# Optimization experiments

Measured on AMD Instinct MI355X. Metric: run time of the kernel, lower is better.

The kernel has to match this reference:

```python
import jax, jax.numpy as jnp
import numpy as np

N_NODES = 40000
N_EDGES = 640000
DIM = 128
N_BASIS = 50
N_FILTERS = 128
CUTOFF = 5.0
LOG2 = float(np.log(2.0))
PI = float(np.pi)


def ssp(t):
    # ShiftedSoftplus: softplus(x) - log(2), numerically stable via logaddexp
    return jnp.logaddexp(t, 0.0) - LOG2


def setup_inputs() -> dict:
    key = jax.random.key(0)
    ks = jax.random.split(key, 16)
    u = lambda k, shape, fan_in: jax.random.uniform(k, shape, jnp.float32, -1.0, 1.0) / np.sqrt(fan_in)
    return {
        "x": jax.random.normal(ks[0], (N_NODES, DIM), jnp.float32),
        "r_ij": jax.random.uniform(ks[1], (N_EDGES,), jnp.float32) * CUTOFF,
        "f_ij": jax.random.normal(ks[2], (N_EDGES, N_BASIS), jnp.float32),
        "ind_i": jax.random.randint(ks[3], (N_EDGES,), 0, N_NODES),
        "ind_j": jax.random.randint(ks[4], (N_EDGES,), 0, N_NODES),
        # parameters
        "W_in2f": u(ks[5], (DIM, N_FILTERS), DIM),            # Linear(dim, n_filters, bias=False)
        "W_f1": u(ks[6], (N_BASIS, N_FILTERS), N_BASIS),       # filter_network Linear 1
        "b_f1": u(ks[7], (N_FILTERS,), N_BASIS),
        "W_f2": u(ks[8], (N_FILTERS, N_FILTERS), N_FILTERS),   # filter_network Linear 2
        "b_f2": u(ks[9], (N_FILTERS,), N_FILTERS),
        "W_out": u(ks[10], (N_FILTERS, DIM), N_FILTERS),       # f2out Linear
        "b_out": u(ks[11], (DIM,), N_FILTERS),
        "W_lin": u(ks[12], (DIM, DIM), DIM),                   # final lin
        "b_lin": u(ks[13], (DIM,), DIM),
    }


def reference(x, r_ij, f_ij, ind_i, ind_j,
              W_in2f, W_f1, b_f1, W_f2, b_f2, W_out, b_out, W_lin, b_lin):
    # filter network: Linear -> ShiftedSoftplus -> Linear, on edges: [E, nf]
    W = ssp(f_ij @ W_f1 + b_f1) @ W_f2 + b_f2
    # cosine cutoff: [E]
    C = 0.5 * (jnp.cos(r_ij * (PI / CUTOFF)) + 1.0) * (r_ij < CUTOFF).astype(r_ij.dtype)
    W = W * C[:, None]
    # node embedding -> filters: [N, nf]
    h = x @ W_in2f
    # gather source nodes, modulate by filters: [E, nf]
    msg = h[ind_j] * W
    # scatter-add pool to destination nodes: [N, nf]
    agg = jax.ops.segment_sum(msg, ind_i, num_segments=x.shape[0])
    # f2out: Linear -> ShiftedSoftplus, then final Linear
    v = ssp(agg @ W_out + b_out)
    return v @ W_lin + b_lin
```

## Files before the change

kernel.cpp:

```cpp
#include <hip/hip_runtime.h>
#include <hip/hip_fp16.h>

#define N_NODES_C 40000
#define N_EDGES_C 640000
#define DIM 128
#define NB 50
#define LDA 132
#define BLK 256
#define TROWS 64
#define LOG2_C 0.6931471805599453f
#define PI_OVER_CUT 0.6283185307179586f
#define NSCAN_BLK 157

typedef __attribute__((ext_vector_type(8))) short s8v;
typedef __attribute__((ext_vector_type(4))) float f4v;

#define MFMA_BF16 __builtin_amdgcn_mfma_f32_16x16x32_bf16

#define SEG_IN2F_H 0
#define SEG_IN2F_L 20480
#define SEG_F1_H   40960
#define SEG_F1_L   51200
#define SEG_F2_H   61440
#define SEG_F2_L   81920
#define SEG_OUT_H  102400
#define SEG_OUT_L  122880
#define SEG_LIN_H  143360
#define SEG_LIN_L  163840
#define WSPLIT_USHORTS 184320

__device__ __forceinline__ unsigned short f2bf(float x) {
    unsigned int u = __float_as_uint(x);
    u += 0x7fffu + ((u >> 16) & 1u);
    return (unsigned short)(u >> 16);
}
__device__ __forceinline__ float bf2f(unsigned short h) {
    return __uint_as_float(((unsigned int)h) << 16);
}
__device__ __forceinline__ float ssp_f(float t) {
    float e = __expf(-fabsf(t));
    return fmaxf(t, 0.0f) + __logf(1.0f + e) - LOG2_C;
}
__device__ __forceinline__ void split8t(const float* av, s8v& Ah, s8v& Al) {
#pragma unroll
    for (int j = 0; j < 8; j += 2) {
        unsigned int u0 = __float_as_uint(av[j]);
        unsigned int u1 = __float_as_uint(av[j + 1]);
        float h0 = __uint_as_float(u0 & 0xffff0000u);
        float h1 = __uint_as_float(u1 & 0xffff0000u);
        unsigned int r0 = __float_as_uint(av[j] - h0);
        unsigned int r1 = __float_as_uint(av[j + 1] - h1);
        ((unsigned int*)&Ah)[j >> 1] = __builtin_amdgcn_perm(u1, u0, 0x07060302);
        ((unsigned int*)&Al)[j >> 1] = __builtin_amdgcn_perm(r1, r0, 0x07060302);
    }
}
__device__ __forceinline__ void mfma8(const unsigned short* __restrict__ bh,
                                      const unsigned short* __restrict__ bl,
                                      const s8v& Ah, const s8v& Al, f4v acc[8]) {
    s8v B[8];
#pragma unroll
    for (int t = 0; t < 8; ++t) B[t] = *(const s8v*)(bl + t * 640);
#pragma unroll
    for (int t = 0; t < 8; ++t) acc[t] = MFMA_BF16(Ah, B[t], acc[t], 0, 0, 0);
#pragma unroll
    for (int t = 0; t < 8; ++t) B[t] = *(const s8v*)(bh + t * 640);
#pragma unroll
    for (int t = 0; t < 8; ++t) {
        acc[t] = MFMA_BF16(Al, B[t], acc[t], 0, 0, 0);
        acc[t] = MFMA_BF16(Ah, B[t], acc[t], 0, 0, 0);
    }
}

__global__ __launch_bounds__(BLK) void split5_kernel(const float* __restrict__ Wa,
                                                     const float* __restrict__ Wb,
                                                     const float* __restrict__ Wc,
                                                     const float* __restrict__ Wd,
                                                     const float* __restrict__ We,
                                                     unsigned short* __restrict__ Ws) {
    int i = blockIdx.x * BLK + threadIdx.x;
    if (i >= 18 * 4096) return;
    int chunk = i >> 12, r = i & 4095, k = r & 31, col = r >> 5;
    const float* W; int Kr, ck, hb, lb;
    if (chunk < 4)       { W = Wa; Kr = 128; ck = chunk;      hb = SEG_IN2F_H; lb = SEG_IN2F_L; }
    else if (chunk < 6)  { W = Wb; Kr = 50;  ck = chunk - 4;  hb = SEG_F1_H;   lb = SEG_F1_L; }
    else if (chunk < 10) { W = Wc; Kr = 128; ck = chunk - 6;  hb = SEG_F2_H;   lb = SEG_F2_L; }
    else if (chunk < 14) { W = Wd; Kr = 128; ck = chunk - 10; hb = SEG_OUT_H;  lb = SEG_OUT_L; }
    else                 { W = We; Kr = 128; ck = chunk - 14; hb = SEG_LIN_H;  lb = SEG_LIN_L; }
    int krow = ck * 32 + k;
    float v = (krow < Kr) ? W[(size_t)krow * DIM + col] : 0.f;
    unsigned short h16 = f2bf(v);
    int o = ck * 5120 + col * 40 + k;
    Ws[hb + o] = h16;
    Ws[lb + o] = f2bf(v - bf2f(h16));
}

__global__ __launch_bounds__(BLK, 4) void node_in2f_mfma(const float* __restrict__ x,
                                                         const unsigned short* __restrict__ Ws,
                                                         float* __restrict__ h) {
    const int tid = threadIdx.x;
    const int w = tid >> 6, l = tid & 63, lr = l & 15, lk = l >> 4;
    const int n0 = blockIdx.x * TROWS;
    const int rowA = 16 * w + lr;
    const float* xr = x + (size_t)(n0 + rowA) * DIM;

    f4v acc[8];
#pragma unroll
    for (int t = 0; t < 8; ++t) acc[t] = (f4v){0.f, 0.f, 0.f, 0.f};
#pragma unroll
    for (int kc = 0; kc < 4; ++kc) {
        const float* ap = xr + kc * 32 + lk * 8;
        float4 a0 = *(const float4*)ap, a1 = *(const float4*)(ap + 4);
        float av[8] = {a0.x, a0.y, a0.z, a0.w, a1.x, a1.y, a1.z, a1.w};
        s8v Ah, Al; split8t(av, Ah, Al);
        const int bo = kc * 5120 + lr * 40 + lk * 8;
        mfma8(Ws + SEG_IN2F_H + bo, Ws + SEG_IN2F_L + bo, Ah, Al, acc);
    }
#pragma unroll
    for (int t = 0; t < 8; ++t)
#pragma unroll
        for (int r = 0; r < 4; ++r)
            h[(size_t)(n0 + 16 * w + lk * 4 + r) * DIM + t * 16 + lr] = acc[t][r];
}

__global__ __launch_bounds__(BLK) void hist_kernel(const int* __restrict__ ind_i,
                                                   int* __restrict__ cnt) {
    int e = blockIdx.x * BLK + threadIdx.x;
    if (e < N_EDGES_C) atomicAdd(&cnt[ind_i[e]], 1);
}

__global__ __launch_bounds__(BLK) void scan1_kernel(const int* __restrict__ cnt,
                                                    int* __restrict__ excl,
                                                    int* __restrict__ bsum) {
    __shared__ int s[BLK];
    const int tid = threadIdx.x;
    const int idx = blockIdx.x * BLK + tid;
    int v = (idx < N_NODES_C) ? cnt[idx] : 0;
    s[tid] = v;
    __syncthreads();
    for (int off = 1; off < BLK; off <<= 1) {
        int t = (tid >= off) ? s[tid - off] : 0;
        __syncthreads();
        s[tid] += t;
        __syncthreads();
    }
    if (idx < N_NODES_C) excl[idx] = s[tid] - v;
    if (tid == BLK - 1) bsum[blockIdx.x] = s[tid];
}

__global__ __launch_bounds__(BLK) void scan2_kernel(int* __restrict__ bsum) {
    __shared__ int s[BLK];
    const int tid = threadIdx.x;
    int v = (tid < NSCAN_BLK) ? bsum[tid] : 0;
    s[tid] = v;
    __syncthreads();
    for (int off = 1; off < BLK; off <<= 1) {
        int t = (tid >= off) ? s[tid - off] : 0;
        __syncthreads();
        s[tid] += t;
        __syncthreads();
    }
    if (tid < NSCAN_BLK) bsum[tid] = s[tid] - v;
}

__global__ __launch_bounds__(BLK) void scan3_kernel(int* __restrict__ start,
                                                    int* __restrict__ cursor,
                                                    const int* __restrict__ bsum) {
    const int idx = blockIdx.x * BLK + threadIdx.x;
    if (idx < N_NODES_C) {
        int v = start[idx] + bsum[blockIdx.x];
        start[idx] = v;
        cursor[idx] = v;
    }
}

__global__ __launch_bounds__(BLK) void place_kernel(const int* __restrict__ ind_i,
                                                    int* __restrict__ cursor,
                                                    int* __restrict__ pos) {
    int e = blockIdx.x * BLK + threadIdx.x;
    if (e < N_EDGES_C) {
        int slot = atomicAdd(&cursor[ind_i[e]], 1);
        pos[e] = slot;
    }
}

__global__ __launch_bounds__(BLK, 4) void edge_kernel_mfma(const float* __restrict__ f_ij,
                                                           const float* __restrict__ r_ij,
                                                           const int* __restrict__ ind_j,
                                                           const int* __restrict__ pos,
                                                           const unsigned short* __restrict__ Ws,
                                                           const float* __restrict__ b_f1,
                                                           const float* __restrict__ b_f2,
                                                           const float* __restrict__ h,
                                                           __half* __restrict__ msg) {
    __shared__ __align__(16) char smem[34816];
    unsigned short* t1h = (unsigned short*)smem;
    unsigned short* t1l = t1h + 64 * 136;
    float* tf = (float*)smem;

    const int tid = threadIdx.x;
    const int w = tid >> 6, l = tid & 63, lr = l & 15, lk = l >> 4;
    const int rt = tid >> 4, ct = tid & 15;
    const int e0 = blockIdx.x * TROWS;
    const int rowA = 16 * w + lr;

    f4v acc[8];
#pragma unroll
    for (int t = 0; t < 8; ++t) { float bv = b_f1[t * 16 + lr]; acc[t] = (f4v){bv, bv, bv, bv}; }
    const float* fr = f_ij + (size_t)(e0 + rowA) * NB;
#pragma unroll
    for (int kc = 0; kc < 2; ++kc) {
        int kb = kc * 32 + lk * 8;
        float av[8];
#pragma unroll
        for (int ii = 0; ii < 4; ++ii) {
            int k = kb + ii * 2;
            float2 v = (k < NB) ? *(const float2*)(fr + k) : make_float2(0.f, 0.f);
            av[ii * 2] = v.x; av[ii * 2 + 1] = v.y;
        }
        s8v Ah, Al; split8t(av, Ah, Al);
        const int bo = kc * 5120 + lr * 40 + lk * 8;
        mfma8(Ws + SEG_F1_H + bo, Ws + SEG_F1_L + bo, Ah, Al, acc);
    }
#pragma unroll
    for (int t = 0; t < 8; ++t)
#pragma unroll
        for (int r = 0; r < 4; ++r) {
            float v = ssp_f(acc[t][r]);
            unsigned int u = __float_as_uint(v);
            float hf = __uint_as_float(u & 0xffff0000u);
            int idx = (16 * w + lk * 4 + r) * 136 + t * 16 + lr;
            t1h[idx] = (unsigned short)(u >> 16);
            t1l[idx] = (unsigned short)(__float_as_uint(v - hf) >> 16);
        }
    __syncthreads();

#pragma unroll
    for (int t = 0; t < 8; ++t) { float bv = b_f2[t * 16 + lr]; acc[t] = (f4v){bv, bv, bv, bv}; }
#pragma unroll
    for (int kc = 0; kc < 4; ++kc) {
        s8v Ah = *(const s8v*)&t1h[rowA * 136 + kc * 32 + lk * 8];
        s8v Al = *(const s8v*)&t1l[rowA * 136 + kc * 32 + lk * 8];
        const int bo = kc * 5120 + lr * 40 + lk * 8;
        mfma8(Ws + SEG_F2_H + bo, Ws + SEG_F2_L + bo, Ah, Al, acc);
    }
    __syncthreads();
#pragma unroll
    for (int t = 0; t < 8; ++t)
#pragma unroll
        for (int r = 0; r < 4; ++r)
            tf[(16 * w + lk * 4 + r) * LDA + t * 16 + lr] = acc[t][r];
    __syncthreads();

#pragma unroll
    for (int i = 0; i < 4; ++i) {
        int e = e0 + rt * 4 + i;
        float rr = r_ij[e];
        float C = (rr < 5.0f) ? (0.5f * __cosf(rr * PI_OVER_CUT) + 0.5f) : 0.0f;
        int nj = ind_j[e];
        const float* hp = &h[(size_t)nj * DIM + ct * 8];
        float4 h0 = *(const float4*)hp, h1 = *(const float4*)(hp + 4);
        const float* ep = &tf[(rt * 4 + i) * LDA + ct * 8];
        float4 a0 = *(const float4*)ep, a1 = *(const float4*)(ep + 4);
        __half2 o0 = __floats2half2_rn(h0.x * a0.x * C, h0.y * a0.y * C);
        __half2 o1 = __floats2half2_rn(h0.z * a0.z * C, h0.w * a0.w * C);
        __half2 o2 = __floats2half2_rn(h1.x * a1.x * C, h1.y * a1.y * C);
        __half2 o3 = __floats2half2_rn(h1.z * a1.z * C, h1.w * a1.w * C);
        __half* mp = &msg[(size_t)pos[e] * DIM + ct * 8];
        *(uint4*)mp = make_uint4(*(unsigned int*)&o0, *(unsigned int*)&o1,
                                 *(unsigned int*)&o2, *(unsigned int*)&o3);
    }
}

__global__ __launch_bounds__(BLK) void gather_kernel(const __half* __restrict__ msg,
                                                     const int* __restrict__ start,
                                                     const int* __restrict__ cnt,
                                                     float* __restrict__ agg) {
    const int wave = threadIdx.x >> 6;
    const int lane = threadIdx.x & 63;
    const int node = blockIdx.x * 4 + wave;
    if (node >= N_NODES_C) return;
    const int s = start[node];
    const int d = cnt[node];
    const __half* base = msg + (size_t)s * DIM + lane * 2;
    float ax = 0.f, ay = 0.f;
    int k = 0;
    for (; k + 1 < d; k += 2) {
        float2 fa = __half22float2(*(const __half2*)(base + (size_t)k * DIM));
        float2 fb = __half22float2(*(const __half2*)(base + (size_t)(k + 1) * DIM));
        ax += fa.x + fb.x;
        ay += fa.y + fb.y;
    }
    if (k < d) {
        float2 fa = __half22float2(*(const __half2*)(base + (size_t)k * DIM));
        ax += fa.x;
        ay += fa.y;
    }
    *(float2*)&agg[(size_t)node * DIM + lane * 2] = make_float2(ax, ay);
}

__global__ __launch_bounds__(BLK, 4) void node_out_mfma(const float* __restrict__ agg,
                                                        const unsigned short* __restrict__ Ws,
                                                        const float* __restrict__ b_out,
                                                        const float* __restrict__ b_lin,
                                                        float* __restrict__ out) {
    __shared__ __align__(16) char smem[34816];
    unsigned short* t1h = (unsigned short*)smem;
    unsigned short* t1l = t1h + 64 * 136;

    const int tid = threadIdx.x;
    const int w = tid >> 6, l = tid & 63, lr = l & 15, lk = l >> 4;
    const int n0 = blockIdx.x * TROWS;
    const int rowA = 16 * w + lr;
    const float* ar = agg + (size_t)(n0 + rowA) * DIM;

    f4v acc[8];
#pragma unroll
    for (int t = 0; t < 8; ++t) { float bv = b_out[t * 16 + lr]; acc[t] = (f4v){bv, bv, bv, bv}; }
#pragma unroll
    for (int kc = 0; kc < 4; ++kc) {
        const float* ap = ar + kc * 32 + lk * 8;
        float4 a0 = *(const float4*)ap, a1 = *(const float4*)(ap + 4);
        float av[8] = {a0.x, a0.y, a0.z, a0.w, a1.x, a1.y, a1.z, a1.w};
        s8v Ah, Al; split8t(av, Ah, Al);
        const int bo = kc * 5120 + lr * 40 + lk * 8;
        mfma8(Ws + SEG_OUT_H + bo, Ws + SEG_OUT_L + bo, Ah, Al, acc);
    }
#pragma unroll
    for (int t = 0; t < 8; ++t)
#pragma unroll
        for (int r = 0; r < 4; ++r) {
            float v = ssp_f(acc[t][r]);
            unsigned int u = __float_as_uint(v);
            float hf = __uint_as_float(u & 0xffff0000u);
            int idx = (16 * w + lk * 4 + r) * 136 + t * 16 + lr;
            t1h[idx] = (unsigned short)(u >> 16);
            t1l[idx] = (unsigned short)(__float_as_uint(v - hf) >> 16);
        }
    __syncthreads();

#pragma unroll
    for (int t = 0; t < 8; ++t) { float bv = b_lin[t * 16 + lr]; acc[t] = (f4v){bv, bv, bv, bv}; }
#pragma unroll
    for (int kc = 0; kc < 4; ++kc) {
        s8v Ah = *(const s8v*)&t1h[rowA * 136 + kc * 32 + lk * 8];
        s8v Al = *(const s8v*)&t1l[rowA * 136 + kc * 32 + lk * 8];
        const int bo = kc * 5120 + lr * 40 + lk * 8;
        mfma8(Ws + SEG_LIN_H + bo, Ws + SEG_LIN_L + bo, Ah, Al, acc);
    }
#pragma unroll
    for (int t = 0; t < 8; ++t)
#pragma unroll
        for (int r = 0; r < 4; ++r)
            out[(size_t)(n0 + 16 * w + lk * 4 + r) * DIM + t * 16 + lr] = acc[t][r];
}

__device__ __forceinline__ void stage_chunk(const float* __restrict__ B, int k0, int rows,
                                            float* __restrict__ Bc, int tid) {
    const int n4 = rows * (DIM / 4);
    const float4* Bg = (const float4*)B + (size_t)k0 * (DIM / 4);
    float4* Bc4 = (float4*)Bc;
    for (int i = tid; i < n4; i += BLK) Bc4[i] = Bg[i];
}

__device__ __forceinline__ void init_acc_bias(float acc[4][8], const float* __restrict__ b, int ct) {
    float4 bb0 = *(const float4*)&b[ct * 8];
    float4 bb1 = *(const float4*)&b[ct * 8 + 4];
#pragma unroll
    for (int i = 0; i < 4; ++i) {
        acc[i][0] = bb0.x; acc[i][1] = bb0.y; acc[i][2] = bb0.z; acc[i][3] = bb0.w;
        acc[i][4] = bb1.x; acc[i][5] = bb1.y; acc[i][6] = bb1.z; acc[i][7] = bb1.w;
    }
}

template <int KPAD>
__device__ __forceinline__ void gemm_tile(const float* __restrict__ A_lds, int lda,
                                          const float* __restrict__ Bglob,
                                          float* __restrict__ Bc,
                                          float acc[4][8], int rt, int ct, int tid) {
    for (int k0 = 0; k0 < KPAD; k0 += 32) {
        __syncthreads();
        stage_chunk(Bglob, k0, 32, Bc, tid);
        __syncthreads();
#pragma unroll 2
        for (int k4 = 0; k4 < 8; ++k4) {
            float4 av[4];
#pragma unroll
            for (int i = 0; i < 4; ++i)
                av[i] = *(const float4*)&A_lds[(rt * 4 + i) * lda + k0 + k4 * 4];
#pragma unroll
            for (int kk = 0; kk < 4; ++kk) {
                const float* bp = &Bc[(k4 * 4 + kk) * DIM + ct * 8];
                float4 b0 = *(const float4*)bp;
                float4 b1 = *(const float4*)(bp + 4);
#pragma unroll
                for (int i = 0; i < 4; ++i) {
                    float a = ((const float*)&av[i])[kk];
                    acc[i][0] = fmaf(a, b0.x, acc[i][0]);
                    acc[i][1] = fmaf(a, b0.y, acc[i][1]);
                    acc[i][2] = fmaf(a, b0.z, acc[i][2]);
                    acc[i][3] = fmaf(a, b0.w, acc[i][3]);
                    acc[i][4] = fmaf(a, b1.x, acc[i][4]);
                    acc[i][5] = fmaf(a, b1.y, acc[i][5]);
                    acc[i][6] = fmaf(a, b1.z, acc[i][6]);
                    acc[i][7] = fmaf(a, b1.w, acc[i][7]);
                }
            }
        }
    }
}

template <int NK2>
__device__ __forceinline__ void gemm1_direct(const float* const (&frow)[4], int k2base,
                                             const float* __restrict__ Bc,
                                             float acc[4][8], int ct) {
#pragma unroll 4
    for (int k2 = 0; k2 < NK2; ++k2) {
        float2 a2[4];
#pragma unroll
        for (int i = 0; i < 4; ++i)
            a2[i] = *(const float2*)(frow[i] + (k2base + k2) * 2);
#pragma unroll
        for (int kk = 0; kk < 2; ++kk) {
            const float* bp = &Bc[(k2 * 2 + kk) * DIM + ct * 8];
            float4 b0 = *(const float4*)bp;
            float4 b1 = *(const float4*)(bp + 4);
#pragma unroll
            for (int i = 0; i < 4; ++i) {
                float a = kk ? a2[i].y : a2[i].x;
                acc[i][0] = fmaf(a, b0.x, acc[i][0]);
                acc[i][1] = fmaf(a, b0.y, acc[i][1]);
                acc[i][2] = fmaf(a, b0.z, acc[i][2]);
                acc[i][3] = fmaf(a, b0.w, acc[i][3]);
                acc[i][4] = fmaf(a, b1.x, acc[i][4]);
                acc[i][5] = fmaf(a, b1.y, acc[i][5]);
                acc[i][6] = fmaf(a, b1.z, acc[i][6]);
                acc[i][7] = fmaf(a, b1.w, acc[i][7]);
            }
        }
    }
}

__global__ __launch_bounds__(BLK) void node_in2f_fb(const float* __restrict__ x,
                                                    const float* __restrict__ W,
                                                    float* __restrict__ h) {
    __shared__ float At[TROWS * LDA];
    __shared__ float Bc[32 * DIM];
    const int tid = threadIdx.x;
    const int rt = tid >> 4, ct = tid & 15;
    const int n0 = blockIdx.x * TROWS;
    for (int i = tid; i < TROWS * (DIM / 4); i += BLK) {
        int row = i >> 5, c4 = i & 31;
        *(float4*)&At[row * LDA + c4 * 4] = *(const float4*)&x[(size_t)(n0 + row) * DIM + c4 * 4];
    }
    float acc[4][8];
#pragma unroll
    for (int i = 0; i < 4; ++i)
#pragma unroll
        for (int j = 0; j < 8; ++j) acc[i][j] = 0.f;
    gemm_tile<DIM>(At, LDA, W, Bc, acc, rt, ct, tid);
#pragma unroll
    for (int i = 0; i < 4; ++i) {
        float* hp = &h[(size_t)(n0 + rt * 4 + i) * DIM + ct * 8];
        *(float4*)hp = make_float4(acc[i][0], acc[i][1], acc[i][2], acc[i][3]);
        *(float4*)(hp + 4) = make_float4(acc[i][4], acc[i][5], acc[i][6], acc[i][7]);
    }
}

__global__ __launch_bounds__(BLK) void node_out_fb(const float* __restrict__ agg,
                                                   const float* __restrict__ W_out,
                                                   const float* __restrict__ b_out,
                                                   const float* __restrict__ W_lin,
                                                   const float* __restrict__ b_lin,
                                                   float* __restrict__ out) {
    __shared__ float At[TROWS * LDA];
    __shared__ float Bc[32 * DIM];
    const int tid = threadIdx.x;
    const int rt = tid >> 4, ct = tid & 15;
    const int n0 = blockIdx.x * TROWS;
    for (int i = tid; i < TROWS * (DIM / 4); i += BLK) {
        int row = i >> 5, c4 = i & 31;
        *(float4*)&At[row * LDA + c4 * 4] = *(const float4*)&agg[(size_t)(n0 + row) * DIM + c4 * 4];
    }
    float acc[4][8];
    init_acc_bias(acc, b_out, ct);
    gemm_tile<DIM>(At, LDA, W_out, Bc, acc, rt, ct, tid);
    __syncthreads();
#pragma unroll
    for (int i = 0; i < 4; ++i) {
        float* tp = &At[(rt * 4 + i) * LDA + ct * 8];
        *(float4*)tp = make_float4(ssp_f(acc[i][0]), ssp_f(acc[i][1]),
                                   ssp_f(acc[i][2]), ssp_f(acc[i][3]));
        *(float4*)(tp + 4) = make_float4(ssp_f(acc[i][4]), ssp_f(acc[i][5]),
                                         ssp_f(acc[i][6]), ssp_f(acc[i][7]));
    }
    init_acc_bias(acc, b_lin, ct);
    gemm_tile<DIM>(At, LDA, W_lin, Bc, acc, rt, ct, tid);
#pragma unroll
    for (int i = 0; i < 4; ++i) {
        float* op = &out[(size_t)(n0 + rt * 4 + i) * DIM + ct * 8];
        *(float4*)op = make_float4(acc[i][0], acc[i][1], acc[i][2], acc[i][3]);
        *(float4*)(op + 4) = make_float4(acc[i][4], acc[i][5], acc[i][6], acc[i][7]);
    }
}

__global__ __launch_bounds__(BLK) void edge_kernel_atomic(const float* __restrict__ f_ij,
                                                          const float* __restrict__ r_ij,
                                                          const int* __restrict__ ind_i,
                                                          const int* __restrict__ ind_j,
                                                          const float* __restrict__ W_f1,
                                                          const float* __restrict__ b_f1,
                                                          const float* __restrict__ W_f2,
                                                          const float* __restrict__ b_f2,
                                                          const float* __restrict__ h,
                                                          float* __restrict__ agg) {
    __shared__ float t1[TROWS * LDA];
    __shared__ float Bc[32 * DIM];
    const int tid = threadIdx.x;
    const int rt = tid >> 4, ct = tid & 15;
    const int e0 = blockIdx.x * TROWS;
    const float* frow[4];
#pragma unroll
    for (int i = 0; i < 4; ++i) frow[i] = f_ij + (size_t)(e0 + rt * 4 + i) * NB;
    float acc[4][8];
    init_acc_bias(acc, b_f1, ct);
    stage_chunk(W_f1, 0, 32, Bc, tid);
    __syncthreads();
    gemm1_direct<16>(frow, 0, Bc, acc, ct);
    __syncthreads();
    stage_chunk(W_f1, 32, 18, Bc, tid);
    __syncthreads();
    gemm1_direct<9>(frow, 16, Bc, acc, ct);
#pragma unroll
    for (int i = 0; i < 4; ++i) {
        float* tp = &t1[(rt * 4 + i) * LDA + ct * 8];
        *(float4*)tp = make_float4(ssp_f(acc[i][0]), ssp_f(acc[i][1]),
                                   ssp_f(acc[i][2]), ssp_f(acc[i][3]));
        *(float4*)(tp + 4) = make_float4(ssp_f(acc[i][4]), ssp_f(acc[i][5]),
                                         ssp_f(acc[i][6]), ssp_f(acc[i][7]));
    }
    init_acc_bias(acc, b_f2, ct);
    gemm_tile<DIM>(t1, LDA, W_f2, Bc, acc, rt, ct, tid);
#pragma unroll
    for (int i = 0; i < 4; ++i) {
        int e = e0 + rt * 4 + i;
        float r = r_ij[e];
        float C = (r < 5.0f) ? 0.5f * (cosf(r * PI_OVER_CUT) + 1.0f) : 0.0f;
        int nj = ind_j[e];
        int ni = ind_i[e];
        const float* hp = &h[(size_t)nj * DIM + ct * 8];
        float4 h0 = *(const float4*)hp;
        float4 h1 = *(const float4*)(hp + 4);
        float* ap = &agg[(size_t)ni * DIM + ct * 8];
        atomicAdd(ap + 0, h0.x * acc[i][0] * C);
        atomicAdd(ap + 1, h0.y * acc[i][1] * C);
        atomicAdd(ap + 2, h0.z * acc[i][2] * C);
        atomicAdd(ap + 3, h0.w * acc[i][3] * C);
        atomicAdd(ap + 4, h1.x * acc[i][4] * C);
        atomicAdd(ap + 5, h1.y * acc[i][5] * C);
        atomicAdd(ap + 6, h1.z * acc[i][6] * C);
        atomicAdd(ap + 7, h1.w * acc[i][7] * C);
    }
}

extern "C" void kernel_launch(void* const* d_in, const int* in_sizes, int n_in,
                              void* d_out, int out_size, void* d_ws, size_t ws_size,
                              hipStream_t stream) {
    const float* x      = (const float*)d_in[0];
    const float* r_ij   = (const float*)d_in[1];
    const float* f_ij   = (const float*)d_in[2];
    const int*   ind_i  = (const int*)d_in[3];
    const int*   ind_j  = (const int*)d_in[4];
    const float* W_in2f = (const float*)d_in[5];
    const float* W_f1   = (const float*)d_in[6];
    const float* b_f1   = (const float*)d_in[7];
    const float* W_f2   = (const float*)d_in[8];
    const float* b_f2   = (const float*)d_in[9];
    const float* W_out  = (const float*)d_in[10];
    const float* b_out  = (const float*)d_in[11];
    const float* W_lin  = (const float*)d_in[12];
    const float* b_lin  = (const float*)d_in[13];
    float* out = (float*)d_out;

    char* ws = (char*)d_ws;
    size_t off = 0;
    auto alloc = [&](size_t bytes) {
        char* p = ws + off;
        off = (off + bytes + 511) & ~(size_t)511;
        return p;
    };
    unsigned short* Wsplit = (unsigned short*)alloc(WSPLIT_USHORTS * sizeof(unsigned short));
    float*  h      = (float*)alloc((size_t)N_NODES_C * DIM * sizeof(float));
    float*  agg    = (float*)alloc((size_t)N_NODES_C * DIM * sizeof(float));
    __half* msg    = (__half*)alloc((size_t)N_EDGES_C * DIM * sizeof(__half));
    int*    pos    = (int*)alloc((size_t)N_EDGES_C * sizeof(int));
    int*    cnt    = (int*)alloc((size_t)N_NODES_C * sizeof(int));
    int*    startA = (int*)alloc((size_t)N_NODES_C * sizeof(int));
    int*    cursor = (int*)alloc((size_t)N_NODES_C * sizeof(int));
    int*    bsum   = (int*)alloc((size_t)NSCAN_BLK * sizeof(int));
    const bool have_ws = (off <= ws_size);

    if (have_ws) {
        split5_kernel<<<(18 * 4096 + BLK - 1) / BLK, BLK, 0, stream>>>(
            W_in2f, W_f1, W_f2, W_out, W_lin, Wsplit);

        node_in2f_mfma<<<N_NODES_C / TROWS, BLK, 0, stream>>>(x, Wsplit, h);

        hipMemsetAsync(cnt, 0, (size_t)N_NODES_C * sizeof(int), stream);
        hist_kernel<<<(N_EDGES_C + BLK - 1) / BLK, BLK, 0, stream>>>(ind_i, cnt);
        scan1_kernel<<<NSCAN_BLK, BLK, 0, stream>>>(cnt, startA, bsum);
        scan2_kernel<<<1, BLK, 0, stream>>>(bsum);
        scan3_kernel<<<NSCAN_BLK, BLK, 0, stream>>>(startA, cursor, bsum);
        place_kernel<<<(N_EDGES_C + BLK - 1) / BLK, BLK, 0, stream>>>(ind_i, cursor, pos);

        edge_kernel_mfma<<<N_EDGES_C / TROWS, BLK, 0, stream>>>(
            f_ij, r_ij, ind_j, pos, Wsplit, b_f1, b_f2, h, msg);
        gather_kernel<<<(N_NODES_C + 3) / 4, BLK, 0, stream>>>(msg, startA, cnt, agg);

        node_out_mfma<<<N_NODES_C / TROWS, BLK, 0, stream>>>(agg, Wsplit, b_out, b_lin, out);
    } else {
        float* h2   = (float*)d_ws;
        float* agg2 = h2 + (size_t)N_NODES_C * DIM;
        node_in2f_fb<<<N_NODES_C / TROWS, BLK, 0, stream>>>(x, W_in2f, h2);
        hipMemsetAsync(agg2, 0, (size_t)N_NODES_C * DIM * sizeof(float), stream);
        edge_kernel_atomic<<<N_EDGES_C / TROWS, BLK, 0, stream>>>(
            f_ij, r_ij, ind_i, ind_j, W_f1, b_f1, W_f2, b_f2, h2, agg2);
        node_out_fb<<<N_NODES_C / TROWS, BLK, 0, stream>>>(agg2, W_out, b_out, W_lin, b_lin, out);
    }
}
```

Baseline: 358.6 us.

## Retile MFMA warps to 32x64 output tiles to halve weight fragment loads

Each wave now computes two 16-row blocks across 64 columns instead of one 16-row block across all 128 columns. This lets every B-fragment load from the split-bf16 weight array feed two A tiles, halving per-wave weight traffic in the in2f, filter-network and output GEMM kernels. In exchange each wave loads two A rows per k-chunk and performs two hi/lo splits, which raises register pressure somewhat.

```diff
diff --git a/kernel.cpp b/kernel.cpp
--- a/kernel.cpp
+++ b/kernel.cpp
@@ -54,20 +54,27 @@
         ((unsigned int*)&Al)[j >> 1] = __builtin_amdgcn_perm(r1, r0, 0x07060302);
     }
 }
-__device__ __forceinline__ void mfma8(const unsigned short* __restrict__ bh,
-                                      const unsigned short* __restrict__ bl,
-                                      const s8v& Ah, const s8v& Al, f4v acc[8]) {
-    s8v B[8];
-#pragma unroll
-    for (int t = 0; t < 8; ++t) B[t] = *(const s8v*)(bl + t * 640);
-#pragma unroll
-    for (int t = 0; t < 8; ++t) acc[t] = MFMA_BF16(Ah, B[t], acc[t], 0, 0, 0);
-#pragma unroll
-    for (int t = 0; t < 8; ++t) B[t] = *(const s8v*)(bh + t * 640);
-#pragma unroll
-    for (int t = 0; t < 8; ++t) {
-        acc[t] = MFMA_BF16(Al, B[t], acc[t], 0, 0, 0);
-        acc[t] = MFMA_BF16(Ah, B[t], acc[t], 0, 0, 0);
+__device__ __forceinline__ void mfma4x2(const unsigned short* __restrict__ bh,
+                                        const unsigned short* __restrict__ bl,
+                                        const s8v& Ah0, const s8v& Al0,
+                                        const s8v& Ah1, const s8v& Al1,
+                                        f4v acc0[4], f4v acc1[4]) {
+    s8v B[4];
+#pragma unroll
+    for (int t = 0; t < 4; ++t) B[t] = *(const s8v*)(bl + t * 640);
+#pragma unroll
+    for (int t = 0; t < 4; ++t) {
+        acc0[t] = MFMA_BF16(Ah0, B[t], acc0[t], 0, 0, 0);
+        acc1[t] = MFMA_BF16(Ah1, B[t], acc1[t], 0, 0, 0);
+    }
+#pragma unroll
+    for (int t = 0; t < 4; ++t) B[t] = *(const s8v*)(bh + t * 640);
+#pragma unroll
+    for (int t = 0; t < 4; ++t) {
+        acc0[t] = MFMA_BF16(Al0, B[t], acc0[t], 0, 0, 0);
+        acc0[t] = MFMA_BF16(Ah0, B[t], acc0[t], 0, 0, 0);
+        acc1[t] = MFMA_BF16(Al1, B[t], acc1[t], 0, 0, 0);
+        acc1[t] = MFMA_BF16(Ah1, B[t], acc1[t], 0, 0, 0);
     }
 }
 
@@ -99,27 +106,40 @@
                                                          float* __restrict__ h) {
     const int tid = threadIdx.x;
     const int w = tid >> 6, l = tid & 63, lr = l & 15, lk = l >> 4;
+    const int rpair = w & 1, colbase = (w >> 1) * 64;
     const int n0 = blockIdx.x * TROWS;
-    const int rowA = 16 * w + lr;
-    const float* xr = x + (size_t)(n0 + rowA) * DIM;
-
-    f4v acc[8];
-#pragma unroll
-    for (int t = 0; t < 8; ++t) acc[t] = (f4v){0.f, 0.f, 0.f, 0.f};
+    const int rowA0 = rpair * 32 + lr, rowA1 = rowA0 + 16;
+    const float* xr0 = x + (size_t)(n0 + rowA0) * DIM;
+    const float* xr1 = x + (size_t)(n0 + rowA1) * DIM;
+
+    f4v acc0[4], acc1[4];
+#pragma unroll
+    for (int t = 0; t < 4; ++t) {
+        acc0[t] = (f4v){0.f, 0.f, 0.f, 0.f};
+        acc1[t] = (f4v){0.f, 0.f, 0.f, 0.f};
+    }
 #pragma unroll
     for (int kc = 0; kc < 4; ++kc) {
-        const float* ap = xr + kc * 32 + lk * 8;
-        float4 a0 = *(const float4*)ap, a1 = *(const float4*)(ap + 4);
-        float av[8] = {a0.x, a0.y, a0.z, a0.w, a1.x, a1.y, a1.z, a1.w};
-        s8v Ah, Al; split8t(av, Ah, Al);
-        const int bo = kc * 5120 + lr * 40 + lk * 8;
-        mfma8(Ws + SEG_IN2F_H + bo, Ws + SEG_IN2F_L + bo, Ah, Al, acc);
-    }
-#pragma unroll
-    for (int t = 0; t < 8; ++t)
-#pragma unroll
-        for (int r = 0; r < 4; ++r)
-            h[(size_t)(n0 + 16 * w + lk * 4 + r) * DIM + t * 16 + lr] = acc[t][r];
+        const float* ap0 = xr0 + kc * 32 + lk * 8;
+        const float* ap1 = xr1 + kc * 32 + lk * 8;
+        float4 a0 = *(const float4*)ap0, a1 = *(const float4*)(ap0 + 4);
+        float4 b0 = *(const float4*)ap1, b1 = *(const float4*)(ap1 + 4);
+        float av0[8] = {a0.x, a0.y, a0.z, a0.w, a1.x, a1.y, a1.z, a1.w};
+        float av1[8] = {b0.x, b0.y, b0.z, b0.w, b1.x, b1.y, b1.z, b1.w};
+        s8v Ah0, Al0, Ah1, Al1;
+        split8t(av0, Ah0, Al0);
+        split8t(av1, Ah1, Al1);
+        const int bo = kc * 5120 + (colbase + lr) * 40 + lk * 8;
+        mfma4x2(Ws + SEG_IN2F_H + bo, Ws + SEG_IN2F_L + bo, Ah0, Al0, Ah1, Al1, acc0, acc1);
+    }
+#pragma unroll
+    for (int t = 0; t < 4; ++t)
+#pragma unroll
+        for (int r = 0; r < 4; ++r) {
+            int col = colbase + t * 16 + lr;
+            h[(size_t)(n0 + rpair * 32 + lk * 4 + r) * DIM + col] = acc0[t][r];
+            h[(size_t)(n0 + rpair * 32 + 16 + lk * 4 + r) * DIM + col] = acc1[t][r];
+        }
 }
 
 __global__ __launch_bounds__(BLK) void hist_kernel(const int* __restrict__ ind_i,
@@ -200,55 +220,85 @@
     const int tid = threadIdx.x;
     const int w = tid >> 6, l = tid & 63, lr = l & 15, lk = l >> 4;
     const int rt = tid >> 4, ct = tid & 15;
+    const int rpair = w & 1, colbase = (w >> 1) * 64;
     const int e0 = blockIdx.x * TROWS;
-    const int rowA = 16 * w + lr;
-
-    f4v acc[8];
-#pragma unroll
-    for (int t = 0; t < 8; ++t) { float bv = b_f1[t * 16 + lr]; acc[t] = (f4v){bv, bv, bv, bv}; }
-    const float* fr = f_ij + (size_t)(e0 + rowA) * NB;
+    const int rowA0 = rpair * 32 + lr, rowA1 = rowA0 + 16;
+
+    f4v acc0[4], acc1[4];
+#pragma unroll
+    for (int t = 0; t < 4; ++t) {
+        float bv = b_f1[colbase + t * 16 + lr];
+        acc0[t] = (f4v){bv, bv, bv, bv};
+        acc1[t] = (f4v){bv, bv, bv, bv};
+    }
+    const float* fr0 = f_ij + (size_t)(e0 + rowA0) * NB;
+    const float* fr1 = f_ij + (size_t)(e0 + rowA1) * NB;
 #pragma unroll
     for (int kc = 0; kc < 2; ++kc) {
         int kb = kc * 32 + lk * 8;
-        float av[8];
+        float av0[8], av1[8];
 #pragma unroll
         for (int ii = 0; ii < 4; ++ii) {
             int k = kb + ii * 2;
-            float2 v = (k < NB) ? *(const float2*)(fr + k) : make_float2(0.f, 0.f);
-            av[ii * 2] = v.x; av[ii * 2 + 1] = v.y;
+            float2 v0 = (k < NB) ? *(const float2*)(fr0 + k) : make_float2(0.f, 0.f);
+            float2 v1 = (k < NB) ? *(const float2*)(fr1 + k) : make_float2(0.f, 0.f);
+            av0[ii * 2] = v0.x; av0[ii * 2 + 1] = v0.y;
+            av1[ii * 2] = v1.x; av1[ii * 2 + 1] = v1.y;
         }
-        s8v Ah, Al; split8t(av, Ah, Al);
-        const int bo = kc * 5120 + lr * 40 + lk * 8;
-        mfma8(Ws + SEG_F1_H + bo, Ws + SEG_F1_L + bo, Ah, Al, acc);
-    }
-#pragma unroll
-    for (int t = 0; t < 8; ++t)
+        s8v Ah0, Al0, Ah1, Al1;
+        split8t(av0, Ah0, Al0);
+        split8t(av1, Ah1, Al1);
+        const int bo = kc * 5120 + (colbase + lr) * 40 + lk * 8;
+        mfma4x2(Ws + SEG_F1_H + bo, Ws + SEG_F1_L + bo, Ah0, Al0, Ah1, Al1, acc0, acc1);
+    }
+#pragma unroll
+    for (int t = 0; t < 4; ++t)
 #pragma unroll
         for (int r = 0; r < 4; ++r) {
-            float v = ssp_f(acc[t][r]);
-            unsigned int u = __float_as_uint(v);
-            float hf = __uint_as_float(u & 0xffff0000u);
-            int idx = (16 * w + lk * 4 + r) * 136 + t * 16 + lr;
-            t1h[idx] = (unsigned short)(u >> 16);
-            t1l[idx] = (unsigned short)(__float_as_uint(v - hf) >> 16);
+            int col = colbase + t * 16 + lr;
+            {
+                float v = ssp_f(acc0[t][r]);
+                unsigned int u = __float_as_uint(v);
+                float hf = __uint_as_float(u & 0xffff0000u);
+                int idx = (rpair * 32 + lk * 4 + r) * 136 + col;
+                t1h[idx] = (unsigned short)(u >> 16);
+                t1l[idx] = (unsigned short)(__float_as_uint(v - hf) >> 16);
+            }
+            {
+                float v = ssp_f(acc1[t][r]);
+                unsigned int u = __float_as_uint(v);
+                float hf = __uint_as_float(u & 0xffff0000u);
+                int idx = (rpair * 32 + 16 + lk * 4 + r) * 136 + col;
+                t1h[idx] = (unsigned short)(u >> 16);
+                t1l[idx] = (unsigned short)(__float_as_uint(v - hf) >> 16);
+            }
         }
     __syncthreads();
 
 #pragma unroll
-    for (int t = 0; t < 8; ++t) { float bv = b_f2[t * 16 + lr]; acc[t] = (f4v){bv, bv, bv, bv}; }
+    for (int t = 0; t < 4; ++t) {
+        float bv = b_f2[colbase + t * 16 + lr];
+        acc0[t] = (f4v){bv, bv, bv, bv};
+        acc1[t] = (f4v){bv, bv, bv, bv};
+    }
 #pragma unroll
     for (int kc = 0; kc < 4; ++kc) {
-        s8v Ah = *(const s8v*)&t1h[rowA * 136 + kc * 32 + lk * 8];
-        s8v Al = *(const s8v*)&t1l[rowA * 136 + kc * 32 + lk * 8];
-        const int bo = kc * 5120 + lr * 40 + lk * 8;
-        mfma8(Ws + SEG_F2_H + bo, Ws + SEG_F2_L + bo, Ah, Al, acc);
-    }
-    __syncthreads();
-#pragma unroll
-    for (int t = 0; t < 8; ++t)
-#pragma unroll
-        for (int r = 0; r < 4; ++r)
-            tf[(16 * w + lk * 4 + r) * LDA + t * 16 + lr] = acc[t][r];
+        s8v Ah0 = *(const s8v*)&t1h[rowA0 * 136 + kc * 32 + lk * 8];
+        s8v Al0 = *(const s8v*)&t1l[rowA0 * 136 + kc * 32 + lk * 8];
+        s8v Ah1 = *(const s8v*)&t1h[rowA1 * 136 + kc * 32 + lk * 8];
+        s8v Al1 = *(const s8v*)&t1l[rowA1 * 136 + kc * 32 + lk * 8];
+        const int bo = kc * 5120 + (colbase + lr) * 40 + lk * 8;
+        mfma4x2(Ws + SEG_F2_H + bo, Ws + SEG_F2_L + bo, Ah0, Al0, Ah1, Al1, acc0, acc1);
+    }
+    __syncthreads();
+#pragma unroll
+    for (int t = 0; t < 4; ++t)
+#pragma unroll
+        for (int r = 0; r < 4; ++r) {
+            int col = colbase + t * 16 + lr;
+            tf[(rpair * 32 + lk * 4 + r) * LDA + col] = acc0[t][r];
+            tf[(rpair * 32 + 16 + lk * 4 + r) * LDA + col] = acc1[t][r];
+        }
     __syncthreads();
 
 #pragma unroll
@@ -309,49 +359,80 @@
 
     const int tid = threadIdx.x;
     const int w = tid >> 6, l = tid & 63, lr = l & 15, lk = l >> 4;
+    const int rpair = w & 1, colbase = (w >> 1) * 64;
     const int n0 = blockIdx.x * TROWS;
-    const int rowA = 16 * w + lr;
-    const float* ar = agg + (size_t)(n0 + rowA) * DIM;
-
-    f4v acc[8];
-#pragma unroll
-    for (int t = 0; t < 8; ++t) { float bv = b_out[t * 16 + lr]; acc[t] = (f4v){bv, bv, bv, bv}; }
+    const int rowA0 = rpair * 32 + lr, rowA1 = rowA0 + 16;
+    const float* ar0 = agg + (size_t)(n0 + rowA0) * DIM;
+    const float* ar1 = agg + (size_t)(n0 + rowA1) * DIM;
+
+    f4v acc0[4], acc1[4];
+#pragma unroll
+    for (int t = 0; t < 4; ++t) {
+        float bv = b_out[colbase + t * 16 + lr];
+        acc0[t] = (f4v){bv, bv, bv, bv};
+        acc1[t] = (f4v){bv, bv, bv, bv};
+    }
 #pragma unroll
     for (int kc = 0; kc < 4; ++kc) {
-        const float* ap = ar + kc * 32 + lk * 8;
-        float4 a0 = *(const float4*)ap, a1 = *(const float4*)(ap + 4);
-        float av[8] = {a0.x, a0.y, a0.z, a0.w, a1.x, a1.y, a1.z, a1.w};
-        s8v Ah, Al; split8t(av, Ah, Al);
-        const int bo = kc * 5120 + lr * 40 + lk * 8;
-        mfma8(Ws + SEG_OUT_H + bo, Ws + SEG_OUT_L + bo, Ah, Al, acc);
-    }
-#pragma unroll
-    for (int t = 0; t < 8; ++t)
+        const float* ap0 = ar0 + kc * 32 + lk * 8;
+        const float* ap1 = ar1 + kc * 32 + lk * 8;
+        float4 a0 = *(const float4*)ap0, a1 = *(const float4*)(ap0 + 4);
+        float4 b0 = *(const float4*)ap1, b1 = *(const float4*)(ap1 + 4);
+        float av0[8] = {a0.x, a0.y, a0.z, a0.w, a1.x, a1.y, a1.z, a1.w};
+        float av1[8] = {b0.x, b0.y, b0.z, b0.w, b1.x, b1.y, b1.z, b1.w};
+        s8v Ah0, Al0, Ah1, Al1;
+        split8t(av0, Ah0, Al0);
+        split8t(av1, Ah1, Al1);
+        const int bo = kc * 5120 + (colbase + lr) * 40 + lk * 8;
+        mfma4x2(Ws + SEG_OUT_H + bo, Ws + SEG_OUT_L + bo, Ah0, Al0, Ah1, Al1, acc0, acc1);
+    }
+#pragma unroll
+    for (int t = 0; t < 4; ++t)
 #pragma unroll
         for (int r = 0; r < 4; ++r) {
-            float v = ssp_f(acc[t][r]);
-            unsigned int u = __float_as_uint(v);
-            float hf = __uint_as_float(u & 0xffff0000u);
-            int idx = (16 * w + lk * 4 + r) * 136 + t * 16 + lr;
-            t1h[idx] = (unsigned short)(u >> 16);
-            t1l[idx] = (unsigned short)(__float_as_uint(v - hf) >> 16);
+            int col = colbase + t * 16 + lr;
+            {
+                float v = ssp_f(acc0[t][r]);
+                unsigned int u = __float_as_uint(v);
+                float hf = __uint_as_float(u & 0xffff0000u);
+                int idx = (rpair * 32 + lk * 4 + r) * 136 + col;
+                t1h[idx] = (unsigned short)(u >> 16);
+                t1l[idx] = (unsigned short)(__float_as_uint(v - hf) >> 16);
+            }
+            {
+                float v = ssp_f(acc1[t][r]);
+                unsigned int u = __float_as_uint(v);
+                float hf = __uint_as_float(u & 0xffff0000u);
+                int idx = (rpair * 32 + 16 + lk * 4 + r) * 136 + col;
+                t1h[idx] = (unsigned short)(u >> 16);
+                t1l[idx] = (unsigned short)(__float_as_uint(v - hf) >> 16);
+            }
         }
     __syncthreads();
 
 #pragma unroll
-    for (int t = 0; t < 8; ++t) { float bv = b_lin[t * 16 + lr]; acc[t] = (f4v){bv, bv, bv, bv}; }
+    for (int t = 0; t < 4; ++t) {
+        float bv = b_lin[colbase + t * 16 + lr];
+        acc0[t] = (f4v){bv, bv, bv, bv};
+        acc1[t] = (f4v){bv, bv, bv, bv};
+    }
 #pragma unroll
     for (int kc = 0; kc < 4; ++kc) {
-        s8v Ah = *(const s8v*)&t1h[rowA * 136 + kc * 32 + lk * 8];
-        s8v Al = *(const s8v*)&t1l[rowA * 136 + kc * 32 + lk * 8];
-        const int bo = kc * 5120 + lr * 40 + lk * 8;
-        mfma8(Ws + SEG_LIN_H + bo, Ws + SEG_LIN_L + bo, Ah, Al, acc);
-    }
-#pragma unroll
-    for (int t = 0; t < 8; ++t)
-#pragma unroll
-        for (int r = 0; r < 4; ++r)
-            out[(size_t)(n0 + 16 * w + lk * 4 + r) * DIM + t * 16 + lr] = acc[t][r];
+        s8v Ah0 = *(const s8v*)&t1h[rowA0 * 136 + kc * 32 + lk * 8];
+        s8v Al0 = *(const s8v*)&t1l[rowA0 * 136 + kc * 32 + lk * 8];
+        s8v Ah1 = *(const s8v*)&t1h[rowA1 * 136 + kc * 32 + lk * 8];
+        s8v Al1 = *(const s8v*)&t1l[rowA1 * 136 + kc * 32 + lk * 8];
+        const int bo = kc * 5120 + (colbase + lr) * 40 + lk * 8;
+        mfma4x2(Ws + SEG_LIN_H + bo, Ws + SEG_LIN_L + bo, Ah0, Al0, Ah1, Al1, acc0, acc1);
+    }
+#pragma unroll
+    for (int t = 0; t < 4; ++t)
+#pragma unroll
+        for (int r = 0; r < 4; ++r) {
+            int col = colbase + t * 16 + lr;
+            out[(size_t)(n0 + rpair * 32 + lk * 4 + r) * DIM + col] = acc0[t][r];
+            out[(size_t)(n0 + rpair * 32 + 16 + lk * 4 + r) * DIM + col] = acc1[t][r];
+        }
 }
 
 __device__ __forceinline__ void stage_chunk(const float* __restrict__ B, int k0, int rows,
```

Result: faster. 308.4 us (-14.0%).
